# Kernel tuning notes

Hardware: AMD Instinct MI355X
Metric: run time of the kernel (lower is better)

Reference implementation:

```python
import jax, jax.numpy as jnp
import numpy as np

LN_EPS = 1e-3  # keras LayerNormalization default epsilon
H = 32


def _glorot(key, shape):
    fan_in, fan_out = shape[0], shape[1]
    lim = np.sqrt(6.0 / (fan_in + fan_out)).astype(np.float32)
    return jax.random.uniform(key, shape, jnp.float32, -lim, lim)


def setup_inputs() -> dict:
    key = jax.random.key(0)
    ks = jax.random.split(key, 10)
    ns, nc, d = 4096, 1024, 64
    num_seq, seq_len = 32, 256
    return {
        "sites": jax.random.normal(ks[0], (ns, d), jnp.float32),
        "cons": jax.random.normal(ks[1], (nc, d), jnp.float32),
        "idx_lower": jax.random.randint(ks[2], (ns,), 0, num_seq * seq_len, jnp.int32),
        "idx_higher": jax.random.randint(ks[3], (ns,), 0, num_seq * seq_len, jnp.int32),
        "W_s": _glorot(ks[4], (d, H)), "b_s": jnp.zeros((H,), jnp.float32),
        "W_c": _glorot(ks[5], (d, H)), "b_c": jnp.zeros((H,), jnp.float32),
        "W_d": _glorot(ks[6], (H, H)), "b_d": jnp.zeros((H,), jnp.float32),
        "ln_g": jnp.ones((H,), jnp.float32), "ln_b": jnp.zeros((H,), jnp.float32),
        "W_o": _glorot(ks[7], (H, 1)), "b_o": jnp.zeros((1,), jnp.float32),
        "num_seq": num_seq, "seq_len": seq_len,
    }


def reference(sites, cons, idx_lower, idx_higher, W_s, b_s, W_c, b_c,
              W_d, b_d, ln_g, ln_b, W_o, b_o, num_seq, seq_len):
    s = jax.nn.relu(sites @ W_s + b_s)          # [ns, 32]
    c = jax.nn.relu(cons @ W_c + b_c)           # [nc, 32]
    comb = s[:, None, :] + c[None, :, :]        # [ns, nc, 32] broadcast-sum
    h = comb @ W_d + b_d                        # decoder MLP: Dense(32)
    mu = jnp.mean(h, axis=-1, keepdims=True)
    var = jnp.var(h, axis=-1, keepdims=True)
    h = (h - mu) * jax.lax.rsqrt(var + LN_EPS) * ln_g + ln_b  # LayerNorm
    logits = (h @ W_o + b_o)[..., 0]            # [ns, nc]
    M = jax.nn.softmax(logits, axis=-1)

    nc_ = M.shape[1]
    slots = num_seq * seq_len

    def band(cum, idx):
        # scatter_nd (duplicate indices accumulate) onto slot grid
        Z = jnp.zeros((slots, nc_), M.dtype).at[idx].add(cum)
        Z = Z.reshape(num_seq, seq_len, nc_)
        p = jax.nn.relu(1.0 - Z)
        # exclusive cumprod along the position (seq_len) axis
        excl = jnp.cumprod(
            jnp.concatenate([jnp.ones_like(p[:, :1]), p[:, :-1]], axis=1), axis=1)
        return excl.reshape(slots, nc_)[idx]    # gather back per site

    M_c_lower = jnp.flip(jnp.cumsum(jnp.flip(M, -1), axis=-1), -1)  # reverse cumsum
    M_c_higher = jnp.cumsum(M, axis=-1)
    M_lower = band(M_c_lower, idx_lower)
    M_higher = band(M_c_higher, idx_higher)
    return M * M_lower * M_higher
```

## Files before the change

kernel.cpp:

```cpp
#include <hip/hip_runtime.h>

#define NS 4096
#define NCC 1024
#define DD 64
#define HH2 32
#define NSEQ 32
#define SLEN 256
#define SLOTS 8192
#define LNEPS 1e-3f
#define MAXCH 96

__global__ void __launch_bounds__(1024) k_setup(
    const float* __restrict__ sites, const float* __restrict__ cons,
    const float* __restrict__ Ws, const float* __restrict__ bs,
    const float* __restrict__ Wc, const float* __restrict__ bc,
    const float* __restrict__ Wd, const float* __restrict__ bd,
    const float* __restrict__ g, const float* __restrict__ Wo,
    float* __restrict__ u, float* __restrict__ A, float* __restrict__ P,
    float* __restrict__ v, float* __restrict__ B, float* __restrict__ Q,
    const int* __restrict__ idxl, const int* __restrict__ idxh,
    int* __restrict__ offl, int* __restrict__ slotl, int* __restrict__ sitel,
    int* __restrict__ offh, int* __restrict__ sloth, int* __restrict__ siteh) {
  __shared__ int cnt[SLOTS];
  __shared__ int wsumI[16];
  int tid = threadIdx.x;
  if (blockIdx.x < 20) {
    if (tid >= 256) return;
    int t = blockIdx.x * 256 + tid;
    if (t >= NS + NCC) return;
    bool isSite = t < NS;
    int row = isSite ? t : t - NS;
    const float* x = isSite ? sites + row * DD : cons + row * DD;
    const float* W1 = isSite ? Ws : Wc;
    const float* b1 = isSite ? bs : bc;
    float s[HH2];
#pragma unroll
    for (int h = 0; h < HH2; h++) s[h] = b1[h];
    for (int k = 0; k < DD; k++) {
      float xv = x[k];
#pragma unroll
      for (int h = 0; h < HH2; h++) s[h] = fmaf(xv, W1[k * HH2 + h], s[h]);
    }
#pragma unroll
    for (int h = 0; h < HH2; h++) s[h] = fmaxf(s[h], 0.0f);
    float hs[HH2];
#pragma unroll
    for (int h = 0; h < HH2; h++) hs[h] = isSite ? 0.0f : bd[h];
    for (int k = 0; k < HH2; k++) {
      float sv = s[k];
#pragma unroll
      for (int h = 0; h < HH2; h++) hs[h] = fmaf(sv, Wd[k * HH2 + h], hs[h]);
    }
    float mu = 0.f;
#pragma unroll
    for (int h = 0; h < HH2; h++) mu += hs[h];
    mu *= (1.0f / HH2);
    float p = 0.f, a = 0.f;
    float* dst = isSite ? (u + row * HH2) : (v + row * HH2);
#pragma unroll
    for (int h = 0; h < HH2; h++) {
      float uu = hs[h] - mu;
      dst[h] = uu;
      p += uu * uu;
      a = fmaf(uu * g[h], Wo[h], a);
    }
    p *= (1.0f / HH2);
    if (isSite) { A[row] = a; P[row] = p; } else { B[row] = a; Q[row] = p; }
    return;
  }
  int lane = tid & 63, wv = tid >> 6;
  int pass = blockIdx.x - 20;
  const int* idx = pass ? idxh : idxl;
  int* off = pass ? offh : offl;
  int* slotA = pass ? sloth : slotl;
  int* siteA = pass ? siteh : sitel;
  for (int i2 = tid; i2 < SLOTS; i2 += 1024) cnt[i2] = 0;
  __syncthreads();
  for (int i2 = tid; i2 < NS; i2 += 1024) atomicAdd(&cnt[idx[i2]], 1);
  __syncthreads();
  int base = tid * 8;
  int loc[8]; int sum = 0;
#pragma unroll
  for (int q2 = 0; q2 < 8; q2++) { loc[q2] = sum; sum += cnt[base + q2]; }
  int incl = sum;
#pragma unroll
  for (int o = 1; o < 64; o <<= 1) { int t2 = __shfl_up(incl, o); if (lane >= o) incl += t2; }
  if (lane == 63) wsumI[wv] = incl;
  __syncthreads();
  int wprev = 0;
#pragma unroll
  for (int w = 0; w < 16; w++) { int t3 = wsumI[w]; if (w < wv) wprev += t3; }
  int excl = wprev + (incl - sum);
  __syncthreads();
#pragma unroll
  for (int q2 = 0; q2 < 8; q2++) { int o2 = excl + loc[q2]; off[base + q2] = o2; cnt[base + q2] = o2; }
  if (tid == 0) off[SLOTS] = NS;
  __syncthreads();
  for (int i2 = tid; i2 < NS; i2 += 1024) {
    int sl = idx[i2];
    int pos = atomicAdd(&cnt[sl], 1);
    slotA[pos] = sl; siteA[pos] = i2;
  }
}

__global__ void __launch_bounds__(1024) k_main(const float* __restrict__ u,
    const float* __restrict__ A, const float* __restrict__ P,
    const float* __restrict__ v, const float* __restrict__ B, const float* __restrict__ Q,
    const float* __restrict__ lnb, const float* __restrict__ Wo, const float* __restrict__ bo,
    float* __restrict__ M, float* __restrict__ CLp, float* __restrict__ CHp) {
  int j = threadIdx.x;
  int lane = j & 63, wv = j >> 6;
  __shared__ float redB[16 * 16];
  float4 vv[8];
  const float4* vp = (const float4*)(v + j * HH2);
#pragma unroll
  for (int q = 0; q < 8; q++) vv[q] = vp[q];
  float Bj = B[j], Qj = Q[j];
  float C = bo[0];
#pragma unroll
  for (int k = 0; k < HH2; k++) C = fmaf(lnb[k], Wo[k], C);
  int row0 = blockIdx.x * 16;

  float e[16], incl[16];
#pragma unroll
  for (int rr = 0; rr < 16; rr++) {
    int i = row0 + rr;
    const float4* up = (const float4*)(u + i * HH2);
    float dot = 0.f;
#pragma unroll
    for (int q = 0; q < 8; q++) {
      float4 u4 = up[q];
      dot = fmaf(u4.x, vv[q].x, dot);
      dot = fmaf(u4.y, vv[q].y, dot);
      dot = fmaf(u4.z, vv[q].z, dot);
      dot = fmaf(u4.w, vv[q].w, dot);
    }
    float var = P[i] + Qj + dot * 0.0625f;
    float lg = rsqrtf(var + LNEPS) * (A[i] + Bj) + C;
    float ee = __expf(lg);
    float ic = ee;
#pragma unroll
    for (int o = 1; o < 64; o <<= 1) { float tt = __shfl_up(ic, o); if (lane >= o) ic += tt; }
    if (lane == 63) redB[rr * 16 + wv] = ic;
    e[rr] = ee; incl[rr] = ic;
  }
  __syncthreads();
#pragma unroll
  for (int rr = 0; rr < 16; rr++) {
    const float4* rb = (const float4*)(redB + rr * 16);
    float4 b0 = rb[0], b1 = rb[1], b2 = rb[2], b3 = rb[3];
    float w_[16] = {b0.x, b0.y, b0.z, b0.w, b1.x, b1.y, b1.z, b1.w,
                    b2.x, b2.y, b2.z, b2.w, b3.x, b3.y, b3.z, b3.w};
    float prev = 0.f, tot = 0.f;
#pragma unroll
    for (int w = 0; w < 16; w++) { tot += w_[w]; if (w < wv) prev += w_[w]; }
    float chE = prev + incl[rr];
    float rd = 1.0f / tot;
    int o_ = (row0 + rr) * NCC + j;
    M[o_] = e[rr] * rd;
    CHp[o_] = chE * rd;
    CLp[o_] = (tot - chE + e[rr]) * rd;
  }
}

__global__ void __launch_bounds__(256) k_band(
    float* __restrict__ CLp, float* __restrict__ CHp,
    const int* __restrict__ offl, const int* __restrict__ slotl, const int* __restrict__ sitel,
    const int* __restrict__ offh, const int* __restrict__ sloth, const int* __restrict__ siteh,
    float* __restrict__ TT) {
  int band = blockIdx.y >> 3;
  int chunk = blockIdx.y & 7;
  int seq = blockIdx.z;
  int j = blockIdx.x * 256 + threadIdx.x;
  const int* off = band ? offh : offl;
  const int* slA = band ? sloth : slotl;
  const int* siA = band ? siteh : sitel;
  float* C = band ? CHp : CLp;
  int slot0 = seq * SLEN + chunk * 32;
  int s0 = off[slot0];
  int n = off[slot0 + 32] - s0;
  size_t trow = ((size_t)band * 256 + seq * 8 + chunk) * NCC + j;
  if (n <= 0) { TT[trow] = 1.0f; return; }
  if (n > MAXCH) n = MAXCH;
  __shared__ int ss[MAXCH];
  __shared__ int sl[MAXCH];
  for (int i = threadIdx.x; i < n; i += 256) { ss[i] = siA[s0 + i]; sl[i] = slA[s0 + i]; }
  __syncthreads();

  const int T = 32;
  float buf[T];
#pragma unroll
  for (int k = 0; k < T; k++) {
    int kk = k < n ? k : n - 1;
    buf[k] = C[(size_t)ss[kk] * NCC + j];
  }
  float r = 1.f, z = 0.f;
  int prev = -1;
#pragma unroll
  for (int k = 0; k < T; k++) {
    if (k < n) {
      float cv = buf[k];
      int slot = sl[k];
      if (slot != prev) {
        if (prev >= 0) { r *= fmaxf(1.f - z, 0.f); z = 0.f; }
        prev = slot;
      }
      C[(size_t)ss[k] * NCC + j] = r;
      z += cv;
    }
  }
  for (int k = T; k < n; k++) {
    float cv = C[(size_t)ss[k] * NCC + j];
    int slot = sl[k];
    if (slot != prev) {
      if (prev >= 0) { r *= fmaxf(1.f - z, 0.f); z = 0.f; }
      prev = slot;
    }
    C[(size_t)ss[k] * NCC + j] = r;
    z += cv;
  }
  r *= fmaxf(1.f - z, 0.f);
  TT[trow] = r;
}

__global__ void __launch_bounds__(1024) k_prefix(float* __restrict__ TT) {
  int b = blockIdx.x;
  int j = threadIdx.x;
  float* base = TT + (size_t)b * 8 * NCC + j;
  float t[8];
#pragma unroll
  for (int c = 0; c < 8; c++) t[c] = base[(size_t)c * NCC];
  float p = 1.f;
#pragma unroll
  for (int c = 0; c < 8; c++) { base[(size_t)c * NCC] = p; p *= t[c]; }
}

__global__ void __launch_bounds__(256) k_final(
    float* __restrict__ out, const float* __restrict__ ELr, const float* __restrict__ EHr,
    const float* __restrict__ TT, const int* __restrict__ idxl, const int* __restrict__ idxh) {
  int j = threadIdx.x * 4;
  int s0 = blockIdx.x * 8;
  const float* TTH = TT + (size_t)256 * NCC;
#pragma unroll 4
  for (int k = 0; k < 8; k++) {
    int s = s0 + k;
    size_t bofs = (size_t)s * NCC + j;
    float4 m  = *(const float4*)(out + bofs);
    float4 el = *(const float4*)(ELr + bofs);
    float4 eh = *(const float4*)(EHr + bofs);
    float4 pl = *(const float4*)(TT  + (size_t)(idxl[s] >> 5) * NCC + j);
    float4 ph = *(const float4*)(TTH + (size_t)(idxh[s] >> 5) * NCC + j);
    float4 o;
    o.x = m.x * el.x * pl.x * eh.x * ph.x;
    o.y = m.y * el.y * pl.y * eh.y * ph.y;
    o.z = m.z * el.z * pl.z * eh.z * ph.z;
    o.w = m.w * el.w * pl.w * eh.w * ph.w;
    *(float4*)(out + bofs) = o;
  }
}

extern "C" void kernel_launch(void* const* d_in, const int* in_sizes, int n_in,
                              void* d_out, int out_size, void* d_ws, size_t ws_size,
                              hipStream_t stream) {
  const float* sites = (const float*)d_in[0];
  const float* cons  = (const float*)d_in[1];
  const int* idxl = (const int*)d_in[2];
  const int* idxh = (const int*)d_in[3];
  const float* Ws = (const float*)d_in[4];
  const float* bs = (const float*)d_in[5];
  const float* Wc = (const float*)d_in[6];
  const float* bc = (const float*)d_in[7];
  const float* Wd = (const float*)d_in[8];
  const float* bd = (const float*)d_in[9];
  const float* lng = (const float*)d_in[10];
  const float* lnb = (const float*)d_in[11];
  const float* Wo = (const float*)d_in[12];
  const float* bo = (const float*)d_in[13];

  char* wsb = (char*)d_ws;
  size_t o = 0;
  auto alloc = [&](size_t bytes) { char* p = wsb + o; o += (bytes + 15) & ~(size_t)15; return p; };
  float* u   = (float*)alloc((size_t)NS * HH2 * 4);
  float* A   = (float*)alloc((size_t)NS * 4);
  float* P   = (float*)alloc((size_t)NS * 4);
  float* v   = (float*)alloc((size_t)NCC * HH2 * 4);
  float* B   = (float*)alloc((size_t)NCC * 4);
  float* Q   = (float*)alloc((size_t)NCC * 4);
  float* CLp = (float*)alloc((size_t)NS * NCC * 4);
  float* CHp = (float*)alloc((size_t)NS * NCC * 4);
  float* TT  = (float*)alloc((size_t)2 * 256 * NCC * 4);
  int* offl  = (int*)alloc((SLOTS + 1) * 4);
  int* slotl = (int*)alloc(NS * 4);
  int* sitel = (int*)alloc(NS * 4);
  int* offh  = (int*)alloc((SLOTS + 1) * 4);
  int* sloth = (int*)alloc(NS * 4);
  int* siteh = (int*)alloc(NS * 4);

  k_setup<<<22, 1024, 0, stream>>>(sites, cons, Ws, bs, Wc, bc, Wd, bd, lng, Wo,
                                   u, A, P, v, B, Q,
                                   idxl, idxh, offl, slotl, sitel, offh, sloth, siteh);
  k_main<<<NS / 16, 1024, 0, stream>>>(u, A, P, v, B, Q, lnb, Wo, bo,
                                       (float*)d_out, CLp, CHp);
  k_band<<<dim3(4, 16, 32), 256, 0, stream>>>(CLp, CHp,
                                              offl, slotl, sitel, offh, sloth, siteh, TT);
  k_prefix<<<64, 1024, 0, stream>>>(TT);
  k_final<<<NS / 8, 256, 0, stream>>>((float*)d_out, CLp, CHp, TT, idxl, idxh);
}
```

Baseline: 158.2 us.

## Fuse band, prefix and final kernels into one cooperative kernel with grid syncs

Replaces the three trailing launches (band scan, chunk prefix product, final combine) with a single cooperative kernel of 1024 blocks that uses grid.sync between phases. A fallback to the original three kernels is kept if the cooperative launch fails. The aim is to remove two kernel launch gaps and their tail effects. In exchange it pays for grid-wide barrier cost, and the kernel needs 1024 co-resident blocks (launch bounds 256 threads, 4 blocks per SIMD hint). The prefix phase uses only 256 blocks while the rest wait at the barrier.

After: 410.2 us. 2.59x slower.

```diff
diff --git a/kernel.cpp b/kernel.cpp
--- a/kernel.cpp
+++ b/kernel.cpp
@@ -1,4 +1,7 @@
 #include <hip/hip_runtime.h>
+#include <hip/hip_cooperative_groups.h>
+
+namespace cg = cooperative_groups;
 
 #define NS 4096
 #define NCC 1024
@@ -163,6 +166,108 @@
   }
 }
 
+__global__ void __launch_bounds__(256, 4) k_mega(
+    float* __restrict__ CLp, float* __restrict__ CHp,
+    const int* __restrict__ offl, const int* __restrict__ slotl, const int* __restrict__ sitel,
+    const int* __restrict__ offh, const int* __restrict__ sloth, const int* __restrict__ siteh,
+    float* __restrict__ TT, float* __restrict__ out,
+    const int* __restrict__ idxl, const int* __restrict__ idxh) {
+  cg::grid_group grid = cg::this_grid();
+  int b = blockIdx.x;
+  int tid = threadIdx.x;
+  __shared__ int ss[MAXCH];
+  __shared__ int sl[MAXCH];
+  for (int rnd = 0; rnd < 2; rnd++) {
+    int t = b + rnd * 1024;
+    int coltile = t & 3;
+    int chunk = (t >> 2) & 7;
+    int band = (t >> 5) & 1;
+    int seq = t >> 6;
+    const int* off = band ? offh : offl;
+    const int* slA = band ? sloth : slotl;
+    const int* siA = band ? siteh : sitel;
+    float* Cb = band ? CHp : CLp;
+    int j = coltile * 256 + tid;
+    int slot0 = seq * SLEN + chunk * 32;
+    int s0 = off[slot0];
+    int n = off[slot0 + 32] - s0;
+    size_t trow = ((size_t)band * 256 + seq * 8 + chunk) * NCC + j;
+    __syncthreads();
+    if (n > MAXCH) n = MAXCH;
+    for (int i = tid; i < n; i += 256) { ss[i] = siA[s0 + i]; sl[i] = slA[s0 + i]; }
+    __syncthreads();
+    if (n <= 0) { TT[trow] = 1.0f; continue; }
+
+    const int T = 32;
+    float buf[T];
+#pragma unroll
+    for (int k = 0; k < T; k++) {
+      int kk = k < n ? k : n - 1;
+      buf[k] = Cb[(size_t)ss[kk] * NCC + j];
+    }
+    float r = 1.f, z = 0.f;
+    int prev = -1;
+#pragma unroll
+    for (int k = 0; k < T; k++) {
+      if (k < n) {
+        float cv = buf[k];
+        int slot = sl[k];
+        if (slot != prev) {
+          if (prev >= 0) { r *= fmaxf(1.f - z, 0.f); z = 0.f; }
+          prev = slot;
+        }
+        Cb[(size_t)ss[k] * NCC + j] = r;
+        z += cv;
+      }
+    }
+    for (int k = T; k < n; k++) {
+      float cv = Cb[(size_t)ss[k] * NCC + j];
+      int slot = sl[k];
+      if (slot != prev) {
+        if (prev >= 0) { r *= fmaxf(1.f - z, 0.f); z = 0.f; }
+        prev = slot;
+      }
+      Cb[(size_t)ss[k] * NCC + j] = r;
+      z += cv;
+    }
+    r *= fmaxf(1.f - z, 0.f);
+    TT[trow] = r;
+  }
+  grid.sync();
+  if (b < 256) {
+    int group = b >> 2;
+    int col = (b & 3) * 256 + tid;
+    float* base = TT + (size_t)group * 8 * NCC + col;
+    float t0[8];
+#pragma unroll
+    for (int c = 0; c < 8; c++) t0[c] = base[(size_t)c * NCC];
+    float p = 1.f;
+#pragma unroll
+    for (int c = 0; c < 8; c++) { base[(size_t)c * NCC] = p; p *= t0[c]; }
+  }
+  grid.sync();
+  {
+    int jj = tid * 4;
+    const float* TTH = TT + (size_t)256 * NCC;
+#pragma unroll
+    for (int k = 0; k < 4; k++) {
+      int s = b * 4 + k;
+      size_t bofs = (size_t)s * NCC + jj;
+      float4 m  = *(const float4*)(out + bofs);
+      float4 el = *(const float4*)(CLp + bofs);
+      float4 eh = *(const float4*)(CHp + bofs);
+      float4 pl = *(const float4*)(TT  + (size_t)(idxl[s] >> 5) * NCC + jj);
+      float4 ph = *(const float4*)(TTH + (size_t)(idxh[s] >> 5) * NCC + jj);
+      float4 o;
+      o.x = m.x * el.x * pl.x * eh.x * ph.x;
+      o.y = m.y * el.y * pl.y * eh.y * ph.y;
+      o.z = m.z * el.z * pl.z * eh.z * ph.z;
+      o.w = m.w * el.w * pl.w * eh.w * ph.w;
+      *(float4*)(out + bofs) = o;
+    }
+  }
+}
+
 __global__ void __launch_bounds__(256) k_band(
     float* __restrict__ CLp, float* __restrict__ CHp,
     const int* __restrict__ offl, const int* __restrict__ slotl, const int* __restrict__ sitel,
@@ -186,7 +291,6 @@
   __shared__ int sl[MAXCH];
   for (int i = threadIdx.x; i < n; i += 256) { ss[i] = siA[s0 + i]; sl[i] = slA[s0 + i]; }
   __syncthreads();
-
   const int T = 32;
   float buf[T];
 #pragma unroll
@@ -301,8 +405,18 @@
                                    idxl, idxh, offl, slotl, sitel, offh, sloth, siteh);
   k_main<<<NS / 16, 1024, 0, stream>>>(u, A, P, v, B, Q, lnb, Wo, bo,
                                        (float*)d_out, CLp, CHp);
-  k_band<<<dim3(4, 16, 32), 256, 0, stream>>>(CLp, CHp,
-                                              offl, slotl, sitel, offh, sloth, siteh, TT);
-  k_prefix<<<64, 1024, 0, stream>>>(TT);
-  k_final<<<NS / 8, 256, 0, stream>>>((float*)d_out, CLp, CHp, TT, idxl, idxh);
-}
+
+  float* out_f = (float*)d_out;
+  void* args[] = { &CLp, &CHp,
+                   (void*)&offl, (void*)&slotl, (void*)&sitel,
+                   (void*)&offh, (void*)&sloth, (void*)&siteh,
+                   &TT, &out_f, (void*)&idxl, (void*)&idxh };
+  hipError_t ce = hipLaunchCooperativeKernel((const void*)k_mega, dim3(1024), dim3(256),
+                                             args, 0, stream);
+  if (ce != hipSuccess) {
+    k_band<<<dim3(4, 16, 32), 256, 0, stream>>>(CLp, CHp,
+                                                offl, slotl, sitel, offh, sloth, siteh, TT);
+    k_prefix<<<64, 1024, 0, stream>>>(TT);
+    k_final<<<NS / 8, 256, 0, stream>>>((float*)d_out, CLp, CHp, TT, idxl, idxh);
+  }
+}
```

## Derive softmax and lower cumsum from higher cumsum and fuse band products into output

Applied to the files above, without the earlier changes.

k_main now writes only the normalized forward cumsum. M and the reverse cumsum are reconstructed from adjacent cumsum entries: M[j] = CH[j] - CH[j-1] and CL[j] = 1 - CH[j-1]. The band pass is split into a lower and a higher kernel that each process two columns per thread and write their partial products directly into the output. This drops the separate M and CL buffers and the extra reads in k_final, cutting full-size memory traffic substantially. The cost is some precision loss from subtracting cumsums, two serialized band launches with fewer blocks each, and an extra read-modify-write of the output.

After: 164.1 us. 1.04x slower.

```diff
diff --git a/kernel.cpp b/kernel.cpp
--- a/kernel.cpp
+++ b/kernel.cpp
@@ -107,7 +107,7 @@
     const float* __restrict__ A, const float* __restrict__ P,
     const float* __restrict__ v, const float* __restrict__ B, const float* __restrict__ Q,
     const float* __restrict__ lnb, const float* __restrict__ Wo, const float* __restrict__ bo,
-    float* __restrict__ M, float* __restrict__ CLp, float* __restrict__ CHp) {
+    float* __restrict__ CHp) {
   int j = threadIdx.x;
   int lane = j & 63, wv = j >> 6;
   __shared__ float redB[16 * 16];
@@ -156,71 +156,142 @@
     for (int w = 0; w < 16; w++) { tot += w_[w]; if (w < wv) prev += w_[w]; }
     float chE = prev + incl[rr];
     float rd = 1.0f / tot;
-    int o_ = (row0 + rr) * NCC + j;
-    M[o_] = e[rr] * rd;
-    CHp[o_] = chE * rd;
-    CLp[o_] = (tot - chE + e[rr]) * rd;
-  }
-}
-
-__global__ void __launch_bounds__(256) k_band(
-    float* __restrict__ CLp, float* __restrict__ CHp,
+    CHp[(row0 + rr) * NCC + j] = chE * rd;
+  }
+}
+
+__global__ void __launch_bounds__(256) k_bandL(
+    const float* __restrict__ CHp,
     const int* __restrict__ offl, const int* __restrict__ slotl, const int* __restrict__ sitel,
-    const int* __restrict__ offh, const int* __restrict__ sloth, const int* __restrict__ siteh,
-    float* __restrict__ TT) {
-  int band = blockIdx.y >> 3;
-  int chunk = blockIdx.y & 7;
-  int seq = blockIdx.z;
-  int j = blockIdx.x * 256 + threadIdx.x;
-  const int* off = band ? offh : offl;
-  const int* slA = band ? sloth : slotl;
-  const int* siA = band ? siteh : sitel;
-  float* C = band ? CHp : CLp;
+    float* __restrict__ out, float* __restrict__ TT) {
+  int chunk = blockIdx.y, seq = blockIdx.z;
+  int j0 = blockIdx.x * 512 + threadIdx.x * 2;
   int slot0 = seq * SLEN + chunk * 32;
-  int s0 = off[slot0];
-  int n = off[slot0 + 32] - s0;
-  size_t trow = ((size_t)band * 256 + seq * 8 + chunk) * NCC + j;
-  if (n <= 0) { TT[trow] = 1.0f; return; }
+  int s0 = offl[slot0];
+  int n = offl[slot0 + 32] - s0;
+  size_t trow = (size_t)(seq * 8 + chunk) * NCC + j0;
+  if (n <= 0) { *(float2*)(TT + trow) = make_float2(1.f, 1.f); return; }
   if (n > MAXCH) n = MAXCH;
   __shared__ int ss[MAXCH];
   __shared__ int sl[MAXCH];
-  for (int i = threadIdx.x; i < n; i += 256) { ss[i] = siA[s0 + i]; sl[i] = slA[s0 + i]; }
+  for (int i = threadIdx.x; i < n; i += 256) { ss[i] = sitel[s0 + i]; sl[i] = slotl[s0 + i]; }
   __syncthreads();
 
   const int T = 32;
-  float buf[T];
+  float2 ch[T]; float cm[T];
 #pragma unroll
   for (int k = 0; k < T; k++) {
     int kk = k < n ? k : n - 1;
-    buf[k] = C[(size_t)ss[kk] * NCC + j];
-  }
-  float r = 1.f, z = 0.f;
+    const float* rp = CHp + (size_t)ss[kk] * NCC + j0;
+    ch[k] = *(const float2*)rp;
+    cm[k] = (j0 == 0) ? 0.f : rp[-1];
+  }
+  float2 r = make_float2(1.f, 1.f), z = make_float2(0.f, 0.f);
   int prev = -1;
 #pragma unroll
   for (int k = 0; k < T; k++) {
     if (k < n) {
-      float cv = buf[k];
       int slot = sl[k];
       if (slot != prev) {
-        if (prev >= 0) { r *= fmaxf(1.f - z, 0.f); z = 0.f; }
+        if (prev >= 0) {
+          r.x *= fmaxf(1.f - z.x, 0.f); r.y *= fmaxf(1.f - z.y, 0.f);
+          z = make_float2(0.f, 0.f);
+        }
         prev = slot;
       }
-      C[(size_t)ss[k] * NCC + j] = r;
-      z += cv;
+      float2 o;
+      o.x = (ch[k].x - cm[k]) * r.x;
+      o.y = (ch[k].y - ch[k].x) * r.y;
+      *(float2*)(out + (size_t)ss[k] * NCC + j0) = o;
+      z.x += 1.f - cm[k];
+      z.y += 1.f - ch[k].x;
     }
   }
   for (int k = T; k < n; k++) {
-    float cv = C[(size_t)ss[k] * NCC + j];
+    const float* rp = CHp + (size_t)ss[k] * NCC + j0;
+    float2 c2 = *(const float2*)rp;
+    float cmv = (j0 == 0) ? 0.f : rp[-1];
     int slot = sl[k];
     if (slot != prev) {
-      if (prev >= 0) { r *= fmaxf(1.f - z, 0.f); z = 0.f; }
+      if (prev >= 0) {
+        r.x *= fmaxf(1.f - z.x, 0.f); r.y *= fmaxf(1.f - z.y, 0.f);
+        z = make_float2(0.f, 0.f);
+      }
       prev = slot;
     }
-    C[(size_t)ss[k] * NCC + j] = r;
-    z += cv;
-  }
-  r *= fmaxf(1.f - z, 0.f);
-  TT[trow] = r;
+    float2 o;
+    o.x = (c2.x - cmv) * r.x;
+    o.y = (c2.y - c2.x) * r.y;
+    *(float2*)(out + (size_t)ss[k] * NCC + j0) = o;
+    z.x += 1.f - cmv; z.y += 1.f - c2.x;
+  }
+  r.x *= fmaxf(1.f - z.x, 0.f); r.y *= fmaxf(1.f - z.y, 0.f);
+  *(float2*)(TT + trow) = r;
+}
+
+__global__ void __launch_bounds__(256) k_bandH(
+    const float* __restrict__ CHp,
+    const int* __restrict__ offh, const int* __restrict__ sloth, const int* __restrict__ siteh,
+    float* __restrict__ out, float* __restrict__ TT) {
+  int chunk = blockIdx.y, seq = blockIdx.z;
+  int j0 = blockIdx.x * 512 + threadIdx.x * 2;
+  int slot0 = seq * SLEN + chunk * 32;
+  int s0 = offh[slot0];
+  int n = offh[slot0 + 32] - s0;
+  size_t trow = (size_t)(256 + seq * 8 + chunk) * NCC + j0;
+  if (n <= 0) { *(float2*)(TT + trow) = make_float2(1.f, 1.f); return; }
+  if (n > MAXCH) n = MAXCH;
+  __shared__ int ss[MAXCH];
+  __shared__ int sl[MAXCH];
+  for (int i = threadIdx.x; i < n; i += 256) { ss[i] = siteh[s0 + i]; sl[i] = sloth[s0 + i]; }
+  __syncthreads();
+
+  const int T = 32;
+  float2 ch[T], mo[T];
+#pragma unroll
+  for (int k = 0; k < T; k++) {
+    int kk = k < n ? k : n - 1;
+    ch[k] = *(const float2*)(CHp + (size_t)ss[kk] * NCC + j0);
+    mo[k] = *(const float2*)(out + (size_t)ss[kk] * NCC + j0);
+  }
+  float2 r = make_float2(1.f, 1.f), z = make_float2(0.f, 0.f);
+  int prev = -1;
+#pragma unroll
+  for (int k = 0; k < T; k++) {
+    if (k < n) {
+      int slot = sl[k];
+      if (slot != prev) {
+        if (prev >= 0) {
+          r.x *= fmaxf(1.f - z.x, 0.f); r.y *= fmaxf(1.f - z.y, 0.f);
+          z = make_float2(0.f, 0.f);
+        }
+        prev = slot;
+      }
+      float2 o;
+      o.x = mo[k].x * r.x;
+      o.y = mo[k].y * r.y;
+      *(float2*)(out + (size_t)ss[k] * NCC + j0) = o;
+      z.x += ch[k].x;
+      z.y += ch[k].y;
+    }
+  }
+  for (int k = T; k < n; k++) {
+    float2 c2 = *(const float2*)(CHp + (size_t)ss[k] * NCC + j0);
+    float2 m2 = *(const float2*)(out + (size_t)ss[k] * NCC + j0);
+    int slot = sl[k];
+    if (slot != prev) {
+      if (prev >= 0) {
+        r.x *= fmaxf(1.f - z.x, 0.f); r.y *= fmaxf(1.f - z.y, 0.f);
+        z = make_float2(0.f, 0.f);
+      }
+      prev = slot;
+    }
+    float2 o; o.x = m2.x * r.x; o.y = m2.y * r.y;
+    *(float2*)(out + (size_t)ss[k] * NCC + j0) = o;
+    z.x += c2.x; z.y += c2.y;
+  }
+  r.x *= fmaxf(1.f - z.x, 0.f); r.y *= fmaxf(1.f - z.y, 0.f);
+  *(float2*)(TT + trow) = r;
 }
 
 __global__ void __launch_bounds__(1024) k_prefix(float* __restrict__ TT) {
@@ -236,8 +307,8 @@
 }
 
 __global__ void __launch_bounds__(256) k_final(
-    float* __restrict__ out, const float* __restrict__ ELr, const float* __restrict__ EHr,
-    const float* __restrict__ TT, const int* __restrict__ idxl, const int* __restrict__ idxh) {
+    float* __restrict__ out, const float* __restrict__ TT,
+    const int* __restrict__ idxl, const int* __restrict__ idxh) {
   int j = threadIdx.x * 4;
   int s0 = blockIdx.x * 8;
   const float* TTH = TT + (size_t)256 * NCC;
@@ -246,15 +317,13 @@
     int s = s0 + k;
     size_t bofs = (size_t)s * NCC + j;
     float4 m  = *(const float4*)(out + bofs);
-    float4 el = *(const float4*)(ELr + bofs);
-    float4 eh = *(const float4*)(EHr + bofs);
     float4 pl = *(const float4*)(TT  + (size_t)(idxl[s] >> 5) * NCC + j);
     float4 ph = *(const float4*)(TTH + (size_t)(idxh[s] >> 5) * NCC + j);
     float4 o;
-    o.x = m.x * el.x * pl.x * eh.x * ph.x;
-    o.y = m.y * el.y * pl.y * eh.y * ph.y;
-    o.z = m.z * el.z * pl.z * eh.z * ph.z;
-    o.w = m.w * el.w * pl.w * eh.w * ph.w;
+    o.x = m.x * pl.x * ph.x;
+    o.y = m.y * pl.y * ph.y;
+    o.z = m.z * pl.z * ph.z;
+    o.w = m.w * pl.w * ph.w;
     *(float4*)(out + bofs) = o;
   }
 }
@@ -286,7 +355,6 @@
   float* v   = (float*)alloc((size_t)NCC * HH2 * 4);
   float* B   = (float*)alloc((size_t)NCC * 4);
   float* Q   = (float*)alloc((size_t)NCC * 4);
-  float* CLp = (float*)alloc((size_t)NS * NCC * 4);
   float* CHp = (float*)alloc((size_t)NS * NCC * 4);
   float* TT  = (float*)alloc((size_t)2 * 256 * NCC * 4);
   int* offl  = (int*)alloc((SLOTS + 1) * 4);
@@ -299,10 +367,9 @@
   k_setup<<<22, 1024, 0, stream>>>(sites, cons, Ws, bs, Wc, bc, Wd, bd, lng, Wo,
                                    u, A, P, v, B, Q,
                                    idxl, idxh, offl, slotl, sitel, offh, sloth, siteh);
-  k_main<<<NS / 16, 1024, 0, stream>>>(u, A, P, v, B, Q, lnb, Wo, bo,
-                                       (float*)d_out, CLp, CHp);
-  k_band<<<dim3(4, 16, 32), 256, 0, stream>>>(CLp, CHp,
-                                              offl, slotl, sitel, offh, sloth, siteh, TT);
+  k_main<<<NS / 16, 1024, 0, stream>>>(u, A, P, v, B, Q, lnb, Wo, bo, CHp);
+  k_bandL<<<dim3(2, 8, NSEQ), 256, 0, stream>>>(CHp, offl, slotl, sitel, (float*)d_out, TT);
+  k_bandH<<<dim3(2, 8, NSEQ), 256, 0, stream>>>(CHp, offh, sloth, siteh, (float*)d_out, TT);
   k_prefix<<<64, 1024, 0, stream>>>(TT);
-  k_final<<<NS / 8, 256, 0, stream>>>((float*)d_out, CLp, CHp, TT, idxl, idxh);
-}
+  k_final<<<NS / 8, 256, 0, stream>>>((float*)d_out, TT, idxl, idxh);
+}
```

## Derive M and lower cumsum from inclusive cumsum, drop prefix kernel

Applied to the files above, without the earlier changes.

k_main now writes only the inclusive cumsum array; M and the reverse cumsum are rebuilt in k_band from adjacent cumsum entries (M = ch[j]-ch[j-1], lower = 1-ch[j-1]), and the lower band writes M*E_lower straight into the output. The separate k_prefix launch goes away and k_final computes the chunk prefix product inline by looping over earlier chunk totals. This cuts one full NS×NCC array from both the writes and the reads of the pipeline and removes a kernel launch. In exchange it adds an extra unaligned neighbour load, a variable-length loop in k_final, and possible precision loss from subtracting cumsums.

New measurement: 160.2 us. About the same (+1.2%).

```diff
diff --git a/kernel.cpp b/kernel.cpp
--- a/kernel.cpp
+++ b/kernel.cpp
@@ -107,7 +107,7 @@
     const float* __restrict__ A, const float* __restrict__ P,
     const float* __restrict__ v, const float* __restrict__ B, const float* __restrict__ Q,
     const float* __restrict__ lnb, const float* __restrict__ Wo, const float* __restrict__ bo,
-    float* __restrict__ M, float* __restrict__ CLp, float* __restrict__ CHp) {
+    float* __restrict__ CHp) {
   int j = threadIdx.x;
   int lane = j & 63, wv = j >> 6;
   __shared__ float redB[16 * 16];
@@ -121,7 +121,7 @@
   for (int k = 0; k < HH2; k++) C = fmaf(lnb[k], Wo[k], C);
   int row0 = blockIdx.x * 16;
 
-  float e[16], incl[16];
+  float incl[16];
 #pragma unroll
   for (int rr = 0; rr < 16; rr++) {
     int i = row0 + rr;
@@ -142,7 +142,7 @@
 #pragma unroll
     for (int o = 1; o < 64; o <<= 1) { float tt = __shfl_up(ic, o); if (lane >= o) ic += tt; }
     if (lane == 63) redB[rr * 16 + wv] = ic;
-    e[rr] = ee; incl[rr] = ic;
+    incl[rr] = ic;
   }
   __syncthreads();
 #pragma unroll
@@ -156,26 +156,23 @@
     for (int w = 0; w < 16; w++) { tot += w_[w]; if (w < wv) prev += w_[w]; }
     float chE = prev + incl[rr];
     float rd = 1.0f / tot;
-    int o_ = (row0 + rr) * NCC + j;
-    M[o_] = e[rr] * rd;
-    CHp[o_] = chE * rd;
-    CLp[o_] = (tot - chE + e[rr]) * rd;
+    CHp[(row0 + rr) * NCC + j] = chE * rd;
   }
 }
 
 __global__ void __launch_bounds__(256) k_band(
-    float* __restrict__ CLp, float* __restrict__ CHp,
+    const float* __restrict__ CHp,
     const int* __restrict__ offl, const int* __restrict__ slotl, const int* __restrict__ sitel,
     const int* __restrict__ offh, const int* __restrict__ sloth, const int* __restrict__ siteh,
-    float* __restrict__ TT) {
+    float* __restrict__ outL, float* __restrict__ EHb, float* __restrict__ TT) {
   int band = blockIdx.y >> 3;
   int chunk = blockIdx.y & 7;
   int seq = blockIdx.z;
-  int j = blockIdx.x * 256 + threadIdx.x;
+  int tid = threadIdx.x;
+  int j = blockIdx.x * 256 + tid;
   const int* off = band ? offh : offl;
   const int* slA = band ? sloth : slotl;
   const int* siA = band ? siteh : sitel;
-  float* C = band ? CHp : CLp;
   int slot0 = seq * SLEN + chunk * 32;
   int s0 = off[slot0];
   int n = off[slot0 + 32] - s0;
@@ -184,77 +181,109 @@
   if (n > MAXCH) n = MAXCH;
   __shared__ int ss[MAXCH];
   __shared__ int sl[MAXCH];
-  for (int i = threadIdx.x; i < n; i += 256) { ss[i] = siA[s0 + i]; sl[i] = slA[s0 + i]; }
+  for (int i = tid; i < n; i += 256) { ss[i] = siA[s0 + i]; sl[i] = slA[s0 + i]; }
   __syncthreads();
 
   const int T = 32;
-  float buf[T];
-#pragma unroll
-  for (int k = 0; k < T; k++) {
-    int kk = k < n ? k : n - 1;
-    buf[k] = C[(size_t)ss[kk] * NCC + j];
-  }
   float r = 1.f, z = 0.f;
   int prev = -1;
-#pragma unroll
-  for (int k = 0; k < T; k++) {
-    if (k < n) {
-      float cv = buf[k];
+  if (band == 0) {
+    float ch[T], cm[T];
+#pragma unroll
+    for (int k = 0; k < T; k++) {
+      int kk = k < n ? k : n - 1;
+      const float* rp = CHp + (size_t)ss[kk] * NCC + j;
+      ch[k] = *rp;
+      cm[k] = (j == 0) ? 0.f : rp[-1];
+    }
+#pragma unroll
+    for (int k = 0; k < T; k++) {
+      if (k < n) {
+        int slot = sl[k];
+        if (slot != prev) {
+          if (prev >= 0) { r *= fmaxf(1.f - z, 0.f); z = 0.f; }
+          prev = slot;
+        }
+        outL[(size_t)ss[k] * NCC + j] = (ch[k] - cm[k]) * r;
+        z += 1.f - cm[k];
+      }
+    }
+    for (int k = T; k < n; k++) {
+      const float* rp = CHp + (size_t)ss[k] * NCC + j;
+      float c = *rp, cmv = (j == 0) ? 0.f : rp[-1];
       int slot = sl[k];
       if (slot != prev) {
         if (prev >= 0) { r *= fmaxf(1.f - z, 0.f); z = 0.f; }
         prev = slot;
       }
-      C[(size_t)ss[k] * NCC + j] = r;
-      z += cv;
-    }
-  }
-  for (int k = T; k < n; k++) {
-    float cv = C[(size_t)ss[k] * NCC + j];
-    int slot = sl[k];
-    if (slot != prev) {
-      if (prev >= 0) { r *= fmaxf(1.f - z, 0.f); z = 0.f; }
-      prev = slot;
-    }
-    C[(size_t)ss[k] * NCC + j] = r;
-    z += cv;
+      outL[(size_t)ss[k] * NCC + j] = (c - cmv) * r;
+      z += 1.f - cmv;
+    }
+  } else {
+    float ch[T];
+#pragma unroll
+    for (int k = 0; k < T; k++) {
+      int kk = k < n ? k : n - 1;
+      ch[k] = CHp[(size_t)ss[kk] * NCC + j];
+    }
+#pragma unroll
+    for (int k = 0; k < T; k++) {
+      if (k < n) {
+        int slot = sl[k];
+        if (slot != prev) {
+          if (prev >= 0) { r *= fmaxf(1.f - z, 0.f); z = 0.f; }
+          prev = slot;
+        }
+        EHb[(size_t)ss[k] * NCC + j] = r;
+        z += ch[k];
+      }
+    }
+    for (int k = T; k < n; k++) {
+      float c = CHp[(size_t)ss[k] * NCC + j];
+      int slot = sl[k];
+      if (slot != prev) {
+        if (prev >= 0) { r *= fmaxf(1.f - z, 0.f); z = 0.f; }
+        prev = slot;
+      }
+      EHb[(size_t)ss[k] * NCC + j] = r;
+      z += c;
+    }
   }
   r *= fmaxf(1.f - z, 0.f);
   TT[trow] = r;
 }
 
-__global__ void __launch_bounds__(1024) k_prefix(float* __restrict__ TT) {
-  int b = blockIdx.x;
-  int j = threadIdx.x;
-  float* base = TT + (size_t)b * 8 * NCC + j;
-  float t[8];
-#pragma unroll
-  for (int c = 0; c < 8; c++) t[c] = base[(size_t)c * NCC];
-  float p = 1.f;
-#pragma unroll
-  for (int c = 0; c < 8; c++) { base[(size_t)c * NCC] = p; p *= t[c]; }
-}
-
 __global__ void __launch_bounds__(256) k_final(
-    float* __restrict__ out, const float* __restrict__ ELr, const float* __restrict__ EHr,
-    const float* __restrict__ TT, const int* __restrict__ idxl, const int* __restrict__ idxh) {
+    float* __restrict__ out, const float* __restrict__ EHb, const float* __restrict__ TT,
+    const int* __restrict__ idxl, const int* __restrict__ idxh) {
   int j = threadIdx.x * 4;
   int s0 = blockIdx.x * 8;
   const float* TTH = TT + (size_t)256 * NCC;
-#pragma unroll 4
   for (int k = 0; k < 8; k++) {
     int s = s0 + k;
+    int il = idxl[s] >> 5;
+    int ih = idxh[s] >> 5;
+    int cl = il & 7, chh = ih & 7;
+    const float* tl = TT  + (size_t)(il - cl) * NCC + j;
+    const float* th = TTH + (size_t)(ih - chh) * NCC + j;
+    float4 pl = make_float4(1.f, 1.f, 1.f, 1.f);
+    for (int c = 0; c < cl; c++) {
+      float4 t = *(const float4*)(tl + (size_t)c * NCC);
+      pl.x *= t.x; pl.y *= t.y; pl.z *= t.z; pl.w *= t.w;
+    }
+    float4 ph = make_float4(1.f, 1.f, 1.f, 1.f);
+    for (int c = 0; c < chh; c++) {
+      float4 t = *(const float4*)(th + (size_t)c * NCC);
+      ph.x *= t.x; ph.y *= t.y; ph.z *= t.z; ph.w *= t.w;
+    }
     size_t bofs = (size_t)s * NCC + j;
     float4 m  = *(const float4*)(out + bofs);
-    float4 el = *(const float4*)(ELr + bofs);
-    float4 eh = *(const float4*)(EHr + bofs);
-    float4 pl = *(const float4*)(TT  + (size_t)(idxl[s] >> 5) * NCC + j);
-    float4 ph = *(const float4*)(TTH + (size_t)(idxh[s] >> 5) * NCC + j);
+    float4 eh = *(const float4*)(EHb + bofs);
     float4 o;
-    o.x = m.x * el.x * pl.x * eh.x * ph.x;
-    o.y = m.y * el.y * pl.y * eh.y * ph.y;
-    o.z = m.z * el.z * pl.z * eh.z * ph.z;
-    o.w = m.w * el.w * pl.w * eh.w * ph.w;
+    o.x = m.x * eh.x * pl.x * ph.x;
+    o.y = m.y * eh.y * pl.y * ph.y;
+    o.z = m.z * eh.z * pl.z * ph.z;
+    o.w = m.w * eh.w * pl.w * ph.w;
     *(float4*)(out + bofs) = o;
   }
 }
@@ -286,8 +315,8 @@
   float* v   = (float*)alloc((size_t)NCC * HH2 * 4);
   float* B   = (float*)alloc((size_t)NCC * 4);
   float* Q   = (float*)alloc((size_t)NCC * 4);
-  float* CLp = (float*)alloc((size_t)NS * NCC * 4);
   float* CHp = (float*)alloc((size_t)NS * NCC * 4);
+  float* EHb = (float*)alloc((size_t)NS * NCC * 4);
   float* TT  = (float*)alloc((size_t)2 * 256 * NCC * 4);
   int* offl  = (int*)alloc((SLOTS + 1) * 4);
   int* slotl = (int*)alloc(NS * 4);
@@ -299,10 +328,9 @@
   k_setup<<<22, 1024, 0, stream>>>(sites, cons, Ws, bs, Wc, bc, Wd, bd, lng, Wo,
                                    u, A, P, v, B, Q,
                                    idxl, idxh, offl, slotl, sitel, offh, sloth, siteh);
-  k_main<<<NS / 16, 1024, 0, stream>>>(u, A, P, v, B, Q, lnb, Wo, bo,
-                                       (float*)d_out, CLp, CHp);
-  k_band<<<dim3(4, 16, 32), 256, 0, stream>>>(CLp, CHp,
-                                              offl, slotl, sitel, offh, sloth, siteh, TT);
-  k_prefix<<<64, 1024, 0, stream>>>(TT);
-  k_final<<<NS / 8, 256, 0, stream>>>((float*)d_out, CLp, CHp, TT, idxl, idxh);
-}
+  k_main<<<NS / 16, 1024, 0, stream>>>(u, A, P, v, B, Q, lnb, Wo, bo, CHp);
+  k_band<<<dim3(4, 16, NSEQ), 256, 0, stream>>>(CHp,
+                                                offl, slotl, sitel, offh, sloth, siteh,
+                                                (float*)d_out, EHb, TT);
+  k_final<<<NS / 8, 256, 0, stream>>>((float*)d_out, EHb, TT, idxl, idxh);
+}
```
